# Kernel optimization log

Hardware: AMD Instinct MI355X
Metric: run time of the kernel (lower is better)

The kernel has to match this reference:

```python
import jax, jax.numpy as jnp
from jax import lax
import numpy as np

H = 32  # hidden size
IN = 3  # input dim
NCLASS = 7
T = 30  # sequence length used by forward (indexes t=29)


def _lstm_layer(x, W_ih, W_hh, b_ih, b_hh):
    """One unidirectional LSTM layer, batch_first x: [B,T,D] -> [B,T,H].
    PyTorch gate order: i, f, g, o."""
    B = x.shape[0]
    # Precompute input contribution for all timesteps: [B,T,4H]
    xg = jnp.einsum('btd,gd->btg', x, W_ih) + b_ih + b_hh

    def step(carry, xg_t):
        h, c = carry
        gates = xg_t + h @ W_hh.T  # [B,4H]
        i, f, g, o = jnp.split(gates, 4, axis=-1)
        i = jax.nn.sigmoid(i)
        f = jax.nn.sigmoid(f)
        g = jnp.tanh(g)
        o = jax.nn.sigmoid(o)
        c = f * c + i * g
        h = o * jnp.tanh(c)
        return (h, c), h

    h0 = jnp.zeros((B, H), x.dtype)
    (_, _), hs = lax.scan(step, (h0, h0), jnp.swapaxes(xg, 0, 1))  # hs: [T,B,H]
    return jnp.swapaxes(hs, 0, 1)


def setup_inputs() -> dict:
    key = jax.random.key(0)
    ks = jax.random.split(key, 20)
    B = 65536
    s = 1.0 / np.sqrt(H)  # PyTorch LSTM/Linear init scale
    u = lambda k, shape: jax.random.uniform(k, shape, jnp.float32, -s, s)
    inp = {'X': jax.random.normal(ks[0], (B, T, IN), jnp.float32)}
    dims_in = [IN, H, H]
    for l in range(3):
        inp[f'W_ih{l}'] = u(ks[1 + 4 * l], (4 * H, dims_in[l]))
        inp[f'W_hh{l}'] = u(ks[2 + 4 * l], (4 * H, H))
        inp[f'b_ih{l}'] = u(ks[3 + 4 * l], (4 * H,))
        inp[f'b_hh{l}'] = u(ks[4 + 4 * l], (4 * H,))
    inp['W1'] = u(ks[13], (H // 2, H))
    inp['b1'] = u(ks[14], (H // 2,))
    inp['W2'] = u(ks[15], (NCLASS, H // 2))
    inp['b2'] = u(ks[16], (NCLASS,))
    return inp


def reference(X, W_ih0, W_hh0, b_ih0, b_hh0, W_ih1, W_hh1, b_ih1, b_hh1,
              W_ih2, W_hh2, b_ih2, b_hh2, W1, b1, W2, b2):
    h = _lstm_layer(X, W_ih0, W_hh0, b_ih0, b_hh0)
    h = _lstm_layer(h, W_ih1, W_hh1, b_ih1, b_hh1)
    h = _lstm_layer(h, W_ih2, W_hh2, b_ih2, b_hh2)
    last = h[:, T - 1, :]  # [B,H]
    out = last @ W1.T + b1
    out = out @ W2.T + b2  # [B,7]; Softmax is defined but not applied in forward
    return out
```

## Files before the change

### kernel.cpp

```cpp
#include <hip/hip_runtime.h>
#include <stdint.h>

#define T_STEPS 30
#define BTOT 65536
#define L2E 1.4426950408889634f

typedef __bf16 bf16_t;
typedef bf16_t bf16x8 __attribute__((ext_vector_type(8)));
typedef float f32x4 __attribute__((ext_vector_type(4)));

__device__ __forceinline__ float exp2_fast(float x) {
#if __has_builtin(__builtin_amdgcn_exp2f)
    return __builtin_amdgcn_exp2f(x);
#else
    return __expf(x * 0.6931471805599453f);
#endif
}
__device__ __forceinline__ float rcp_fast(float x) {
    return __builtin_amdgcn_rcpf(x);
}

template <int LI, bool SAVE>
__device__ __forceinline__ void cell(
    int lane, int lrow, int kgrp,
    const bf16_t* __restrict__ wb,
    const float (&bs)[3][8],
    bf16x8 ain,
    bf16x8& ah,
    float (&cst)[3][2][4],
    float (&hsave)[2][4],
    bf16_t* __restrict__ hb)
{
    constexpr int WIH_OFF = ((LI == 0) ? 0 : (LI == 1) ? 2 : 4) * 4096;
    constexpr int WHH_OFF = WIH_OFF + 4096;

    f32x4 z;
    z[0] = 0.0f; z[1] = 0.0f; z[2] = 0.0f; z[3] = 0.0f;
    f32x4 acc[8];
#pragma unroll
    for (int tl = 0; tl < 8; ++tl) {
        bf16x8 bfr = *(const bf16x8*)(wb + WIH_OFF + (tl << 9) + (lane << 3));
        acc[tl] = __builtin_amdgcn_mfma_f32_16x16x32_bf16(ain, bfr, z, 0, 0, 0);
    }
#pragma unroll
    for (int tl = 0; tl < 8; ++tl) {
        bf16x8 bfr = *(const bf16x8*)(wb + WHH_OFF + (tl << 9) + (lane << 3));
        acc[tl] = __builtin_amdgcn_mfma_f32_16x16x32_bf16(ah, bfr, acc[tl], 0, 0, 0);
    }
#pragma unroll
    for (int mt = 0; mt < 2; ++mt) {
#pragma unroll
        for (int r = 0; r < 4; ++r) {
            const float Ae = exp2_fast(acc[0 + mt][r] * (-L2E) + bs[LI][0 + mt]);
            const float Fe = exp2_fast(acc[2 + mt][r] * (-L2E) + bs[LI][2 + mt]);
            const float Be = exp2_fast(acc[4 + mt][r] * (-2.0f * L2E) + bs[LI][4 + mt]);
            const float Oe = exp2_fast(acc[6 + mt][r] * (-L2E) + bs[LI][6 + mt]);
            const float pA = 1.0f + Ae, pF = 1.0f + Fe, pB = 1.0f + Be, pO = 1.0f + Oe;
            const float nB = 1.0f - Be;
            const float t1 = pA * pB;
            const float D  = t1 * pF;
            const float N  = __builtin_fmaf(cst[LI][mt][r], t1, nB * pF);
            const float cc = N * rcp_fast(D);
            cst[LI][mt][r] = cc;
            const float Ce = exp2_fast(cc * (-2.0f * L2E));
            const float pC = 1.0f + Ce, nC = 1.0f - Ce;
            const float hv = nC * rcp_fast(pO * pC);
            if (SAVE) hsave[mt][r] = hv;
            hb[(kgrp * 4 + r) * 40 + mt * 16 + lrow] = (bf16_t)hv;
        }
    }
    ah = *(const bf16x8*)(hb + lrow * 40 + (kgrp << 3));
}

__global__ __launch_bounds__(512, 4) void lstm3_fused(
    const float* __restrict__ X,
    const float* __restrict__ Wih0, const float* __restrict__ Whh0,
    const float* __restrict__ bih0, const float* __restrict__ bhh0,
    const float* __restrict__ Wih1, const float* __restrict__ Whh1,
    const float* __restrict__ bih1, const float* __restrict__ bhh1,
    const float* __restrict__ Wih2, const float* __restrict__ Whh2,
    const float* __restrict__ bih2, const float* __restrict__ bhh2,
    const float* __restrict__ W1, const float* __restrict__ b1,
    const float* __restrict__ W2, const float* __restrict__ b2,
    float* __restrict__ out)
{
    __shared__ alignas(16) bf16_t wfrag[6 * 4096];
    __shared__ float bias_s[3][128];
    __shared__ alignas(16) bf16_t hbuf[8][16 * 40];
    __shared__ float hfin[8][16][33];

    const int tid = threadIdx.x;

    auto stage = [&](int mat, const float* __restrict__ w, int K) {
        for (int p = tid; p < 4096; p += 512) {
            const int tile = p >> 9;
            const int r = p & 511;
            const int ln = r >> 3;
            const int j = r & 7;
            const int k = ((ln >> 4) << 3) + j;
            const int n = (tile << 4) + (ln & 15);
            const float v = (k < K) ? w[n * K + k] : 0.0f;
            wfrag[mat * 4096 + p] = (bf16_t)v;
        }
    };
    stage(0, Wih0, 3);
    stage(1, Whh0, 32);
    stage(2, Wih1, 32);
    stage(3, Whh1, 32);
    stage(4, Wih2, 32);
    stage(5, Whh2, 32);
    for (int p = tid; p < 384; p += 512) {
        const int l = p >> 7, n = p & 127;
        float v;
        if (l == 0)      v = bih0[n] + bhh0[n];
        else if (l == 1) v = bih1[n] + bhh1[n];
        else             v = bih2[n] + bhh2[n];
        bias_s[l][n] = v;
    }
    __syncthreads();

    const int wave = tid >> 6;
    const int lane = tid & 63;
    const int lrow = lane & 15;
    const int kgrp = lane >> 4;
    const int b0   = blockIdx.x * 128 + wave * 16;

    float bs[3][8];
#pragma unroll
    for (int l = 0; l < 3; ++l)
#pragma unroll
        for (int tl = 0; tl < 8; ++tl)
            bs[l][tl] = bias_s[l][tl * 16 + lrow] *
                        (((tl >> 1) == 2) ? (-2.0f * L2E) : (-L2E));

    float cst[3][2][4];
    float h2keep[2][4];
#pragma unroll
    for (int l = 0; l < 3; ++l)
#pragma unroll
        for (int mt = 0; mt < 2; ++mt)
#pragma unroll
            for (int r = 0; r < 4; ++r) cst[l][mt][r] = 0.0f;
#pragma unroll
    for (int mt = 0; mt < 2; ++mt)
#pragma unroll
        for (int r = 0; r < 4; ++r) h2keep[mt][r] = 0.0f;

    bf16x8 ah0, ah1, ah2;
#pragma unroll
    for (int j = 0; j < 8; ++j) {
        ah0[j] = (bf16_t)0.0f; ah1[j] = (bf16_t)0.0f; ah2[j] = (bf16_t)0.0f;
    }

    bf16_t* hb = &hbuf[wave][0];

    const float* xlane = X + (size_t)(b0 + lrow) * (T_STEPS * 3);
    float cx0 = xlane[0], cx1 = xlane[1], cx2 = xlane[2];

    for (int t = 0; t < T_STEPS; ++t) {
        const int tn = (t < T_STEPS - 1) ? (t + 1) : (T_STEPS - 1);
        const float nx0 = xlane[tn * 3 + 0];
        const float nx1 = xlane[tn * 3 + 1];
        const float nx2 = xlane[tn * 3 + 2];

        unsigned lz = 0;
        asm volatile("" : "+v"(lz));
        const bf16_t* wbt = wfrag + lz;

        bf16x8 ax;
#pragma unroll
        for (int j = 0; j < 8; ++j) ax[j] = (bf16_t)0.0f;
        if (kgrp == 0) { ax[0] = (bf16_t)cx0; ax[1] = (bf16_t)cx1; ax[2] = (bf16_t)cx2; }

        cell<0, false>(lane, lrow, kgrp, wbt, bs, ax,  ah0, cst, h2keep, hb);
        cell<1, false>(lane, lrow, kgrp, wbt, bs, ah0, ah1, cst, h2keep, hb);
        cell<2, true >(lane, lrow, kgrp, wbt, bs, ah1, ah2, cst, h2keep, hb);

        cx0 = nx0; cx1 = nx1; cx2 = nx2;
    }

#pragma unroll
    for (int mt = 0; mt < 2; ++mt)
#pragma unroll
        for (int r = 0; r < 4; ++r)
            hfin[wave][kgrp * 4 + r][mt * 16 + lrow] = h2keep[mt][r];

    if (lane < 16) {
        float hv[32];
#pragma unroll
        for (int k = 0; k < 32; ++k) hv[k] = hfin[wave][lane][k];
        float y1[16];
#pragma unroll
        for (int o = 0; o < 16; ++o) {
            float a = b1[o];
#pragma unroll
            for (int k = 0; k < 32; ++k) a += hv[k] * W1[o * 32 + k];
            y1[o] = a;
        }
        const int b = b0 + lane;
#pragma unroll
        for (int q = 0; q < 7; ++q) {
            float a = b2[q];
#pragma unroll
            for (int o = 0; o < 16; ++o) a += y1[o] * W2[q * 16 + o];
            out[b * 7 + q] = a;
        }
    }
}

extern "C" void kernel_launch(void* const* d_in, const int* in_sizes, int n_in,
                              void* d_out, int out_size, void* d_ws, size_t ws_size,
                              hipStream_t stream) {
    (void)in_sizes; (void)n_in; (void)d_ws; (void)ws_size; (void)out_size;
    const float* X    = (const float*)d_in[0];
    const float* Wih0 = (const float*)d_in[1];
    const float* Whh0 = (const float*)d_in[2];
    const float* bih0 = (const float*)d_in[3];
    const float* bhh0 = (const float*)d_in[4];
    const float* Wih1 = (const float*)d_in[5];
    const float* Whh1 = (const float*)d_in[6];
    const float* bih1 = (const float*)d_in[7];
    const float* bhh1 = (const float*)d_in[8];
    const float* Wih2 = (const float*)d_in[9];
    const float* Whh2 = (const float*)d_in[10];
    const float* bih2 = (const float*)d_in[11];
    const float* bhh2 = (const float*)d_in[12];
    const float* W1   = (const float*)d_in[13];
    const float* b1   = (const float*)d_in[14];
    const float* W2   = (const float*)d_in[15];
    const float* b2   = (const float*)d_in[16];
    float* out = (float*)d_out;

    dim3 grid(BTOT / 128), block(512);
    hipLaunchKernelGGL(lstm3_fused, grid, block, 0, stream,
                       X, Wih0, Whh0, bih0, bhh0, Wih1, Whh1, bih1, bhh1,
                       Wih2, Whh2, bih2, bhh2, W1, b1, W2, b2, out);
}
```

Measured before the change: 294.7 us.

## Keep layer-2 recurrent weights in registers and stagger wave start times

```diff
diff --git a/kernel.cpp b/kernel.cpp
--- a/kernel.cpp
+++ b/kernel.cpp
@@ -20,19 +20,24 @@
     return __builtin_amdgcn_rcpf(x);
 }
 
+struct WFrags {
+    bf16x8 f0, f1, f2, f3, f4, f5, f6, f7;
+};
+
 template <int LI, bool SAVE>
 __device__ __forceinline__ void cell(
     int lane, int lrow, int kgrp,
     const bf16_t* __restrict__ wb,
-    const float (&bs)[3][8],
+    const WFrags whh2,
+    const float (&bsL)[8],
     bf16x8 ain,
     bf16x8& ah,
-    float (&cst)[3][2][4],
+    float (&cst)[2][4],
     float (&hsave)[2][4],
     bf16_t* __restrict__ hb)
 {
     constexpr int WIH_OFF = ((LI == 0) ? 0 : (LI == 1) ? 2 : 4) * 4096;
-    constexpr int WHH_OFF = WIH_OFF + 4096;
+    constexpr int WHH_OFF = ((LI == 0) ? 1 : 3) * 4096;
 
     f32x4 z;
     z[0] = 0.0f; z[1] = 0.0f; z[2] = 0.0f; z[3] = 0.0f;
@@ -42,29 +47,39 @@
         bf16x8 bfr = *(const bf16x8*)(wb + WIH_OFF + (tl << 9) + (lane << 3));
         acc[tl] = __builtin_amdgcn_mfma_f32_16x16x32_bf16(ain, bfr, z, 0, 0, 0);
     }
-#pragma unroll
-    for (int tl = 0; tl < 8; ++tl) {
-        bf16x8 bfr = *(const bf16x8*)(wb + WHH_OFF + (tl << 9) + (lane << 3));
-        acc[tl] = __builtin_amdgcn_mfma_f32_16x16x32_bf16(ah, bfr, acc[tl], 0, 0, 0);
+    if constexpr (LI == 2) {
+        acc[0] = __builtin_amdgcn_mfma_f32_16x16x32_bf16(ah, whh2.f0, acc[0], 0, 0, 0);
+        acc[1] = __builtin_amdgcn_mfma_f32_16x16x32_bf16(ah, whh2.f1, acc[1], 0, 0, 0);
+        acc[2] = __builtin_amdgcn_mfma_f32_16x16x32_bf16(ah, whh2.f2, acc[2], 0, 0, 0);
+        acc[3] = __builtin_amdgcn_mfma_f32_16x16x32_bf16(ah, whh2.f3, acc[3], 0, 0, 0);
+        acc[4] = __builtin_amdgcn_mfma_f32_16x16x32_bf16(ah, whh2.f4, acc[4], 0, 0, 0);
+        acc[5] = __builtin_amdgcn_mfma_f32_16x16x32_bf16(ah, whh2.f5, acc[5], 0, 0, 0);
+        acc[6] = __builtin_amdgcn_mfma_f32_16x16x32_bf16(ah, whh2.f6, acc[6], 0, 0, 0);
+        acc[7] = __builtin_amdgcn_mfma_f32_16x16x32_bf16(ah, whh2.f7, acc[7], 0, 0, 0);
+    } else {
+#pragma unroll
+        for (int tl = 0; tl < 8; ++tl) {
+            bf16x8 bfr = *(const bf16x8*)(wb + WHH_OFF + (tl << 9) + (lane << 3));
+            acc[tl] = __builtin_amdgcn_mfma_f32_16x16x32_bf16(ah, bfr, acc[tl], 0, 0, 0);
+        }
     }
 #pragma unroll
     for (int mt = 0; mt < 2; ++mt) {
 #pragma unroll
         for (int r = 0; r < 4; ++r) {
-            const float Ae = exp2_fast(acc[0 + mt][r] * (-L2E) + bs[LI][0 + mt]);
-            const float Fe = exp2_fast(acc[2 + mt][r] * (-L2E) + bs[LI][2 + mt]);
-            const float Be = exp2_fast(acc[4 + mt][r] * (-2.0f * L2E) + bs[LI][4 + mt]);
-            const float Oe = exp2_fast(acc[6 + mt][r] * (-L2E) + bs[LI][6 + mt]);
+            const float Ae = exp2_fast(acc[0 + mt][r] * (-L2E) + bsL[0 + mt]);
+            const float Fe = exp2_fast(acc[2 + mt][r] * (-L2E) + bsL[2 + mt]);
+            const float Be = exp2_fast(acc[4 + mt][r] * (-2.0f * L2E) + bsL[4 + mt]);
+            const float Oe = exp2_fast(acc[6 + mt][r] * (-L2E) + bsL[6 + mt]);
             const float pA = 1.0f + Ae, pF = 1.0f + Fe, pB = 1.0f + Be, pO = 1.0f + Oe;
             const float nB = 1.0f - Be;
             const float t1 = pA * pB;
             const float D  = t1 * pF;
-            const float N  = __builtin_fmaf(cst[LI][mt][r], t1, nB * pF);
+            const float N  = __builtin_fmaf(cst[mt][r], t1, nB * pF);
             const float cc = N * rcp_fast(D);
-            cst[LI][mt][r] = cc;
+            cst[mt][r] = cc;
             const float Ce = exp2_fast(cc * (-2.0f * L2E));
-            const float pC = 1.0f + Ce, nC = 1.0f - Ce;
-            const float hv = nC * rcp_fast(pO * pC);
+            const float hv = (1.0f - Ce) * rcp_fast(pO * (1.0f + Ce));
             if (SAVE) hsave[mt][r] = hv;
             hb[(kgrp * 4 + r) * 40 + mt * 16 + lrow] = (bf16_t)hv;
         }
@@ -84,7 +99,7 @@
     const float* __restrict__ W2, const float* __restrict__ b2,
     float* __restrict__ out)
 {
-    __shared__ alignas(16) bf16_t wfrag[6 * 4096];
+    __shared__ alignas(16) bf16_t wfrag[5 * 4096];
     __shared__ float bias_s[3][128];
     __shared__ alignas(16) bf16_t hbuf[8][16 * 40];
     __shared__ float hfin[8][16][33];
@@ -108,7 +123,6 @@
     stage(2, Wih1, 32);
     stage(3, Whh1, 32);
     stage(4, Wih2, 32);
-    stage(5, Whh2, 32);
     for (int p = tid; p < 384; p += 512) {
         const int l = p >> 7, n = p & 127;
         float v;
@@ -125,6 +139,20 @@
     const int kgrp = lane >> 4;
     const int b0   = blockIdx.x * 128 + wave * 16;
 
+    WFrags whh2;
+    {
+        const float* q = Whh2 + kgrp * 8;
+        auto mk = [&](int tl) {
+            const float* p = q + (tl * 16 + lrow) * 32;
+            bf16x8 f;
+#pragma unroll
+            for (int j = 0; j < 8; ++j) f[j] = (bf16_t)p[j];
+            return f;
+        };
+        whh2.f0 = mk(0); whh2.f1 = mk(1); whh2.f2 = mk(2); whh2.f3 = mk(3);
+        whh2.f4 = mk(4); whh2.f5 = mk(5); whh2.f6 = mk(6); whh2.f7 = mk(7);
+    }
+
     float bs[3][8];
 #pragma unroll
     for (int l = 0; l < 3; ++l)
@@ -132,6 +160,16 @@
         for (int tl = 0; tl < 8; ++tl)
             bs[l][tl] = bias_s[l][tl * 16 + lrow] *
                         (((tl >> 1) == 2) ? (-2.0f * L2E) : (-L2E));
+
+    {
+        const int ph = (((wave >> 2) & 1) << 1) | (blockIdx.x & 1);
+        switch (ph) {
+            case 1: __builtin_amdgcn_s_sleep(25); break;
+            case 2: __builtin_amdgcn_s_sleep(50); break;
+            case 3: __builtin_amdgcn_s_sleep(75); break;
+            default: break;
+        }
+    }
 
     float cst[3][2][4];
     float h2keep[2][4];
@@ -172,9 +210,9 @@
         for (int j = 0; j < 8; ++j) ax[j] = (bf16_t)0.0f;
         if (kgrp == 0) { ax[0] = (bf16_t)cx0; ax[1] = (bf16_t)cx1; ax[2] = (bf16_t)cx2; }
 
-        cell<0, false>(lane, lrow, kgrp, wbt, bs, ax,  ah0, cst, h2keep, hb);
-        cell<1, false>(lane, lrow, kgrp, wbt, bs, ah0, ah1, cst, h2keep, hb);
-        cell<2, true >(lane, lrow, kgrp, wbt, bs, ah1, ah2, cst, h2keep, hb);
+        cell<0, false>(lane, lrow, kgrp, wbt, whh2, bs[0], ax,  ah0, cst[0], h2keep, hb);
+        cell<1, false>(lane, lrow, kgrp, wbt, whh2, bs[1], ah0, ah1, cst[1], h2keep, hb);
+        cell<2, true >(lane, lrow, kgrp, wbt, whh2, bs[2], ah1, ah2, cst[2], h2keep, hb);
 
         cx0 = nx0; cx1 = nx1; cx2 = nx2;
     }
```

Result: slower. 335.4 us (+13.8%).
